# Kernel optimization log

Measured on AMD Instinct MI355X. Metric: run time of the kernel, lower is better.

The kernel has to match this reference:

```python
import jax, jax.numpy as jnp
import numpy as np

EMBED_DIM = 1024
NUM_HEADS = 16
HEAD_DIM = EMBED_DIM // NUM_HEADS
WINDOW = 3
N_RAND = 3
BLOCK = 64
BATCH = 2
SEQ = 2048


def _bigbird_mask(seq_len: int) -> np.ndarray:
    """Global + sliding-window + random block mask. True = attend.
    Deterministic (fixed numpy seed) stand-in for np.random.choice in the
    original; the mask is data-independent so it is a compile-time constant."""
    nb = -(-seq_len // BLOCK)  # ceil division
    mask = np.zeros((seq_len, seq_len), dtype=bool)
    g = min(BLOCK, seq_len)
    mask[:g, :] = True  # global rows
    mask[:, :g] = True  # global cols
    blk = np.arange(seq_len) // BLOCK
    # sliding window: block distance <= WINDOW (matches start/end block loop)
    mask |= np.abs(blk[:, None] - blk[None, :]) <= WINDOW
    rng = np.random.RandomState(0)
    for b in range(1, nb):
        avail = [x for x in range(1, nb) if abs(x - b) > WINDOW]
        if avail:
            sel = rng.choice(avail, size=min(N_RAND, len(avail)), replace=False)
            s0, s1 = b * BLOCK, min(seq_len, (b + 1) * BLOCK)
            for rb in sel:
                mask[s0:s1, rb * BLOCK:min(seq_len, (rb + 1) * BLOCK)] = True
    return mask


def setup_inputs() -> dict:
    key = jax.random.key(0)
    ks = jax.random.split(key, 9)
    E = EMBED_DIM
    std = E ** -0.5
    return {
        "hidden_states": jax.random.normal(ks[0], (BATCH, SEQ, E), jnp.float32),
        "wq": jax.random.normal(ks[1], (E, E), jnp.float32) * std,
        "bq": jnp.zeros((E,), jnp.float32),
        "wk": jax.random.normal(ks[2], (E, E), jnp.float32) * std,
        "bk": jnp.zeros((E,), jnp.float32),
        "wv": jax.random.normal(ks[3], (E, E), jnp.float32) * std,
        "bv": jnp.zeros((E,), jnp.float32),
        "wo": jax.random.normal(ks[4], (E, E), jnp.float32) * std,
        "bo": jnp.zeros((E,), jnp.float32),
    }


def reference(hidden_states, wq, bq, wk, bk, wv, bv, wo, bo):
    B, S, E = hidden_states.shape
    D = HEAD_DIM
    scale = D ** -0.5

    def proj(w, b):  # (B,S,E) -> (B,H,S,D)
        return (hidden_states @ w.T + b).reshape(B, S, NUM_HEADS, D).transpose(0, 2, 1, 3)

    q = proj(wq, bq)
    k = proj(wk, bk)
    v = proj(wv, bv)
    scores = jnp.einsum('bhqd,bhkd->bhqk', q, k) * scale  # dense, masked post-hoc (as in source)
    mask = jnp.asarray(_bigbird_mask(S))
    scores = jnp.where(mask[None, None, :, :], scores, -jnp.inf)
    attn = jax.nn.softmax(scores, axis=-1)
    out = jnp.einsum('bhqk,bhkd->bhqd', attn, v)
    out = out.transpose(0, 2, 1, 3).reshape(B, S, E)
    return out @ wo.T + bo
```

## Files before the change

### kernel.cpp

```cpp
#include <hip/hip_runtime.h>
#include <cstdint>
#include <math.h>


#define DEVI __device__ __forceinline__

typedef __bf16 bf16x8 __attribute__((ext_vector_type(8)));
typedef float floatx4 __attribute__((ext_vector_type(4)));
typedef unsigned short u16x8 __attribute__((ext_vector_type(8)));
typedef unsigned short u16x4 __attribute__((ext_vector_type(4)));
typedef unsigned short ushort_t;

typedef const __attribute__((address_space(1))) void* gptr_as1;
typedef __attribute__((address_space(3))) void* lptr_as3;

DEVI ushort_t f2bf(float f) {
  unsigned u = __float_as_uint(f);
  unsigned r = ((u >> 16) & 1u) + 0x7fffu;
  return (ushort_t)((u + r) >> 16);
}

DEVI void lds_load16(void* lds, const void* g) {
  __builtin_amdgcn_global_load_lds((gptr_as1)g, (lptr_as3)lds, 16, 0, 0);
}

DEVI floatx4 mfma16(bf16x8 a, bf16x8 b, floatx4 c) {
  return __builtin_amdgcn_mfma_f32_16x16x32_bf16(a, b, c, 0, 0, 0);
}

#define BARR() do { asm volatile("" ::: "memory"); \
                    __builtin_amdgcn_s_barrier();  \
                    asm volatile("" ::: "memory"); } while (0)
#define VMC(N) asm volatile("s_waitcnt vmcnt(" #N ")" ::: "memory")

struct MTState { unsigned mt[624]; int mti; };

constexpr unsigned mt_next(MTState& s) {
  if (s.mti >= 624) {
    for (int k = 0; k < 624; ++k) {
      unsigned y = (s.mt[k] & 0x80000000u) | (s.mt[(k + 1) % 624] & 0x7fffffffu);
      unsigned v = s.mt[(k + 397) % 624] ^ (y >> 1);
      if (y & 1u) v ^= 0x9908b0dfu;
      s.mt[k] = v;
    }
    s.mti = 0;
  }
  unsigned y = s.mt[s.mti++];
  y ^= y >> 11;
  y ^= (y << 7) & 0x9d2c5680u;
  y ^= (y << 15) & 0xefc60000u;
  y ^= y >> 18;
  return y;
}

constexpr unsigned mt_interval(MTState& s, unsigned mx) {
  if (mx == 0u) return 0u;
  unsigned msk = mx;
  msk |= msk >> 1; msk |= msk >> 2; msk |= msk >> 4; msk |= msk >> 8; msk |= msk >> 16;
  unsigned v = mt_next(s) & msk;
  while (v > mx) v = mt_next(s) & msk;
  return v;
}

struct MaskPack { unsigned char list[32][32]; int cnt[32]; };

constexpr MaskPack make_pack() {
  unsigned char m[32][32] = {};
  for (int i = 0; i < 32; ++i)
    for (int j = 0; j < 32; ++j) {
      int d = i - j; if (d < 0) d = -d;
      m[i][j] = (i == 0 || j == 0 || d <= 3) ? (unsigned char)1 : (unsigned char)0;
    }
  MTState st{};
  st.mt[0] = 0u;
  for (int i = 1; i < 624; ++i)
    st.mt[i] = 1812433253u * (st.mt[i - 1] ^ (st.mt[i - 1] >> 30)) + (unsigned)i;
  st.mti = 624;
  for (int b = 1; b < 32; ++b) {
    int avail[32] = {}; int n = 0;
    for (int x = 1; x < 32; ++x) {
      int d = x - b; if (d < 0) d = -d;
      if (d > 3) avail[n++] = x;
    }
    if (n == 0) continue;
    int perm[32] = {};
    for (int i = 0; i < n; ++i) perm[i] = i;
    for (int i = n - 1; i > 0; --i) {
      unsigned j = mt_interval(st, (unsigned)i);
      int t = perm[i]; perm[i] = perm[(int)j]; perm[(int)j] = t;
    }
    int take = n < 3 ? n : 3;
    for (int s = 0; s < take; ++s) m[b][avail[perm[s]]] = 1;
  }
  MaskPack P{};
  for (int i = 0; i < 32; ++i) {
    int c = 0;
    for (int j = 0; j < 32; ++j)
      if (m[i][j]) P.list[i][c++] = (unsigned char)j;
    P.cnt[i] = c;
  }
  return P;
}

__constant__ MaskPack MP = make_pack();

__global__ __launch_bounds__(256) void cvt_all(
    const float* __restrict__ hs, const float* __restrict__ wq,
    const float* __restrict__ wk, const float* __restrict__ wv,
    const float* __restrict__ wo,
    ushort_t* __restrict__ hs_bf, ushort_t* __restrict__ wq_bf,
    ushort_t* __restrict__ wk_bf, ushort_t* __restrict__ wv_bf,
    ushort_t* __restrict__ wo_bf) {
  const int i = blockIdx.x * 256 + threadIdx.x;
  const float* s;
  ushort_t* d;
  int j;
  if (i < 1048576) {
    s = hs; d = hs_bf; j = i;
  } else {
    const int t = (i - 1048576) >> 18;
    j = (i - 1048576) & 262143;
    s = t == 0 ? wq : (t == 1 ? wk : (t == 2 ? wv : wo));
    d = t == 0 ? wq_bf : (t == 1 ? wk_bf : (t == 2 ? wv_bf : wo_bf));
  }
  const float4 f = ((const float4*)s)[j];
  u16x4 o;
  o.x = f2bf(f.x); o.y = f2bf(f.y); o.z = f2bf(f.z); o.w = f2bf(f.w);
  ((u16x4*)d)[j] = o;
}

DEVI void stage_half(ushort_t* ldsb, const ushort_t* g, int w, int l) {
  lds_load16(ldsb + w * 1024 + l * 8, g);
  lds_load16(ldsb + w * 1024 + 512 + l * 8, g + 8192);
}

DEVI void rdA(bf16x8 (&a)[4][2], const ushort_t* base, int wm, int li, int quad) {
#pragma unroll
  for (int mi = 0; mi < 4; ++mi) {
    const int rh = wm * 64 + mi * 16 + li;
    const int sw = rh & 7;
#pragma unroll
    for (int ks = 0; ks < 2; ++ks)
      a[mi][ks] = *(const bf16x8*)(base + rh * 64 + (((ks * 4 + quad) ^ sw) << 3));
  }
}

DEVI void rdB(bf16x8 (&b)[2][2], const ushort_t* base, int wn, int li, int quad) {
#pragma unroll
  for (int ni = 0; ni < 2; ++ni) {
    const int rh = wn * 32 + ni * 16 + li;
    const int sw = rh & 7;
#pragma unroll
    for (int ks = 0; ks < 2; ++ks)
      b[ni][ks] = *(const bf16x8*)(base + rh * 64 + (((ks * 4 + quad) ^ sw) << 3));
  }
}

DEVI void mm16(floatx4 (&c)[4][2], const bf16x8 (&a)[4][2], const bf16x8 (&b)[2][2]) {
  __builtin_amdgcn_s_setprio(1);
#pragma unroll
  for (int ks = 0; ks < 2; ++ks)
#pragma unroll
    for (int mi = 0; mi < 4; ++mi)
#pragma unroll
      for (int ni = 0; ni < 2; ++ni)
        c[mi][ni] = mfma16(a[mi][ks], b[ni][ks], c[mi][ni]);
  __builtin_amdgcn_s_setprio(0);
}

__global__ __launch_bounds__(512, 2) void gemm_qkv_fused(
    const ushort_t* __restrict__ A,
    const ushort_t* __restrict__ W0, const ushort_t* __restrict__ W1,
    const ushort_t* __restrict__ W2,
    const float* __restrict__ bq, const float* __restrict__ bk,
    const float* __restrict__ bv,
    ushort_t* __restrict__ Qo, ushort_t* __restrict__ Ko,
    ushort_t* __restrict__ Vt) {
  __shared__ alignas(16) ushort_t LDS[2][2][2][8192];
  const int tid = threadIdx.x;
  const int w = tid >> 6, l = tid & 63, quad = l >> 4, li = l & 15;
  const int wm = w >> 2, wn = w & 3;
  const int bid = blockIdx.x;
  const int swz = (bid & 7) * 24 + (bid >> 3);
  const int m0 = (swz / 12) << 8;
  const int n0g = (swz % 12) << 8;
  const int z = n0g >> 10, n0l = n0g & 1023;
  const ushort_t* Bw = z == 0 ? W0 : (z == 1 ? W1 : W2);
  const float* bias = z == 0 ? bq : (z == 1 ? bk : bv);

  const int rst = w * 16 + (l >> 3);
  const int cst = ((l & 7) ^ (l >> 3)) << 3;
  const ushort_t* gA = A + (size_t)(m0 + rst) * 1024 + cst;
  const ushort_t* gB = Bw + (size_t)(n0l + rst) * 1024 + cst;

  const floatx4 fz = {0.0f, 0.0f, 0.0f, 0.0f};
  floatx4 acc[2][2][4][2];
#pragma unroll
  for (int qm = 0; qm < 2; ++qm)
#pragma unroll
    for (int qn = 0; qn < 2; ++qn)
#pragma unroll
      for (int mi = 0; mi < 4; ++mi)
#pragma unroll
        for (int ni = 0; ni < 2; ++ni) acc[qm][qn][mi][ni] = fz;

  bf16x8 a[4][2], b0[2][2], b1[2][2];

  stage_half(&LDS[0][0][0][0], gA, w, l);
  stage_half(&LDS[0][0][1][0], gA + 131072, w, l);
  stage_half(&LDS[0][1][0][0], gB, w, l);
  stage_half(&LDS[0][1][1][0], gB + 131072, w, l);
  stage_half(&LDS[1][0][0][0], gA + 64, w, l);
  stage_half(&LDS[1][1][0][0], gB + 64, w, l);
  stage_half(&LDS[1][1][1][0], gB + 131072 + 64, w, l);
  VMC(6);
  BARR();

#pragma unroll 1
  for (int it = 0; it < 8; ++it) {
    const bool pf = (it < 7);
    const int o_cy = (2 * it + 1) * 64;
    const int o_x = (2 * it + 2) * 64;
    const int o_y = (2 * it + 3) * 64;

    rdA(a, &LDS[0][0][0][0], wm, li, quad);
    rdB(b0, &LDS[0][1][0][0], wn, li, quad);
    stage_half(&LDS[1][0][1][0], gA + 131072 + o_cy, w, l);
    mm16(acc[0][0], a, b0);
    BARR();

    rdB(b1, &LDS[0][1][1][0], wn, li, quad);
    if (pf) stage_half(&LDS[0][0][0][0], gA + o_x, w, l);
    mm16(acc[0][1], a, b1);
    BARR();

    rdA(a, &LDS[0][0][1][0], wm, li, quad);
    if (pf) stage_half(&LDS[0][1][0][0], gB + o_x, w, l);
    mm16(acc[1][0], a, b0);
    BARR();

    if (pf) stage_half(&LDS[0][1][1][0], gB + 131072 + o_x, w, l);
    mm16(acc[1][1], a, b1);
    if (pf) { VMC(6); } else { VMC(0); }
    BARR();

    rdA(a, &LDS[1][0][0][0], wm, li, quad);
    rdB(b0, &LDS[1][1][0][0], wn, li, quad);
    if (pf) stage_half(&LDS[0][0][1][0], gA + 131072 + o_x, w, l);
    mm16(acc[0][0], a, b0);
    BARR();

    rdB(b1, &LDS[1][1][1][0], wn, li, quad);
    if (pf) stage_half(&LDS[1][0][0][0], gA + o_y, w, l);
    mm16(acc[0][1], a, b1);
    BARR();

    rdA(a, &LDS[1][0][1][0], wm, li, quad);
    if (pf) stage_half(&LDS[1][1][0][0], gB + o_y, w, l);
    mm16(acc[1][0], a, b0);
    BARR();

    if (pf) stage_half(&LDS[1][1][1][0], gB + 131072 + o_y, w, l);
    mm16(acc[1][1], a, b1);
    if (pf) { VMC(6); }
    BARR();
  }

#pragma unroll
  for (int Qm = 0; Qm < 2; ++Qm)
#pragma unroll
    for (int Qn = 0; Qn < 2; ++Qn)
#pragma unroll
      for (int ni = 0; ni < 2; ++ni) {
        const int col = n0l + Qn * 128 + wn * 32 + ni * 16 + li;
        const float bb_ = bias[col];
        if (z == 2) {
          const int hh = col >> 6, dd = col & 63;
#pragma unroll
          for (int mi = 0; mi < 4; ++mi) {
            const int row0 = m0 + Qm * 128 + wm * 64 + mi * 16 + quad * 4;
            const int bb = row0 >> 11, s0 = row0 & 2047;
            u16x4 pk;
#pragma unroll
            for (int r = 0; r < 4; ++r) pk[r] = f2bf(acc[Qm][Qn][mi][ni][r] + bb_);
            *(u16x4*)(Vt + (size_t)((bb * 16 + hh) * 64 + dd) * 2048 + s0) = pk;
          }
        } else {
          ushort_t* Co = (z == 0) ? Qo : Ko;
#pragma unroll
          for (int mi = 0; mi < 4; ++mi)
#pragma unroll
            for (int r = 0; r < 4; ++r) {
              const int row = m0 + Qm * 128 + wm * 64 + mi * 16 + quad * 4 + r;
              Co[(size_t)row * 1024 + col] = f2bf(acc[Qm][Qn][mi][ni][r] + bb_);
            }
        }
      }
}

__global__ __launch_bounds__(256) void gemm_o64(
    const ushort_t* __restrict__ A, const ushort_t* __restrict__ W,
    const float* __restrict__ bias, float* __restrict__ C) {
  constexpr int N = 1024, K = 1024;
  __shared__ alignas(16) ushort_t As[64 * 32];
  __shared__ alignas(16) ushort_t Bs[128 * 32];
  const int tid = threadIdx.x;
  const int w = tid >> 6, l = tid & 63, quad = l >> 4, li = l & 15;
  const int m0 = blockIdx.x * 64, n0 = blockIdx.y * 128;
  const int wm = (w >> 1) * 32, wn = (w & 1) * 64;

  const int lofA = w * 512 + l * 8;
  const int rA = lofA >> 5, cA = lofA & 31;
  const int lofB0 = (w * 2 + 0) * 512 + l * 8;
  const int lofB1 = (w * 2 + 1) * 512 + l * 8;
  const int rB0 = lofB0 >> 5, cB0 = lofB0 & 31;
  const int rB1 = lofB1 >> 5, cB1 = lofB1 & 31;
  const ushort_t* gA = A + (size_t)(m0 + rA) * K + cA;
  const ushort_t* gB0 = W + (size_t)(n0 + rB0) * K + cB0;
  const ushort_t* gB1 = W + (size_t)(n0 + rB1) * K + cB1;

  const floatx4 fzero = {0.0f, 0.0f, 0.0f, 0.0f};
  floatx4 acc[2][4];
#pragma unroll
  for (int i = 0; i < 2; ++i)
#pragma unroll
    for (int j = 0; j < 4; ++j) acc[i][j] = fzero;

  for (int k0 = 0; k0 < K; k0 += 32) {
    lds_load16(As + lofA, gA + k0);
    lds_load16(Bs + lofB0, gB0 + k0);
    lds_load16(Bs + lofB1, gB1 + k0);
    __syncthreads();
    bf16x8 af[2], bfr[4];
#pragma unroll
    for (int mi = 0; mi < 2; ++mi)
      af[mi] = *(const bf16x8*)(As + (wm + mi * 16 + li) * 32 + quad * 8);
#pragma unroll
    for (int ni = 0; ni < 4; ++ni)
      bfr[ni] = *(const bf16x8*)(Bs + (wn + ni * 16 + li) * 32 + quad * 8);
#pragma unroll
    for (int mi = 0; mi < 2; ++mi)
#pragma unroll
      for (int ni = 0; ni < 4; ++ni)
        acc[mi][ni] = mfma16(af[mi], bfr[ni], acc[mi][ni]);
    __syncthreads();
  }

#pragma unroll
  for (int ni = 0; ni < 4; ++ni) {
    const int col = n0 + wn + ni * 16 + li;
    const float bv = bias[col];
#pragma unroll
    for (int mi = 0; mi < 2; ++mi) {
#pragma unroll
      for (int r = 0; r < 4; ++r) {
        const int row = m0 + wm + mi * 16 + quad * 4 + r;
        C[(size_t)row * N + col] = acc[mi][ni][r] + bv;
      }
    }
  }
}

__global__ __launch_bounds__(256) void attn_kernel(
    const ushort_t* __restrict__ Q, const ushort_t* __restrict__ Kg,
    const ushort_t* __restrict__ Vtg, ushort_t* __restrict__ O,
    float* __restrict__ OP, float* __restrict__ LP) {
  __shared__ alignas(16) ushort_t Kls[64 * 72];
  __shared__ alignas(16) ushort_t Vls[64 * 72];
  __shared__ alignas(16) ushort_t Ps[4][16 * 72];

  const int tid = threadIdx.x;
  const int w = tid >> 6, l = tid & 63, quad = l >> 4, li = l & 15;
  const int hb = blockIdx.x;
  const int y = blockIdx.y;
  const bool partial = (y >= 31);
  const int qb = partial ? 0 : (y + 1);
  const int p = partial ? (y - 31) : 0;
  const int base = p * 11;
  const int nact = partial ? (32 - base < 11 ? 32 - base : 11) : MP.cnt[qb];

  const int h = hb & 15, b = hb >> 4;
  const size_t qoff = (size_t)b * 2048 * 1024 + (size_t)h * 64;
  const size_t vtoff = (size_t)hb * 64 * 2048;

  const int qrow = qb * 64 + w * 16 + li;
  bf16x8 aq0 = *(const bf16x8*)(Q + qoff + (size_t)qrow * 1024 + quad * 8);
  bf16x8 aq1 = *(const bf16x8*)(Q + qoff + (size_t)qrow * 1024 + 32 + quad * 8);
#pragma unroll
  for (int j = 0; j < 8; ++j) {
    aq0[j] = (__bf16)((float)aq0[j] * 0.125f);
    aq1[j] = (__bf16)((float)aq1[j] * 0.125f);
  }

  const floatx4 fzero = {0.0f, 0.0f, 0.0f, 0.0f};
  floatx4 o_acc[4];
  float lp[4];
#pragma unroll
  for (int nt = 0; nt < 4; ++nt) o_acc[nt] = fzero;
#pragma unroll
  for (int r = 0; r < 4; ++r) lp[r] = 0.0f;

  const int r0 = w * 16 + (l >> 3);
  const int r1 = r0 + 8;
  const int cb = (l & 7) * 8;
  const ushort_t* kg0 = Kg + qoff + (size_t)r0 * 1024 + cb;
  const ushort_t* kg1 = Kg + qoff + (size_t)r1 * 1024 + cb;
  const ushort_t* vg0 = Vtg + vtoff + (size_t)r0 * 2048 + cb;
  const ushort_t* vg1 = Vtg + vtoff + (size_t)r1 * 2048 + cb;
  ushort_t* kd0 = Kls + r0 * 72 + cb;
  ushort_t* kd1 = Kls + r1 * 72 + cb;
  ushort_t* vd0 = Vls + r0 * 72 + cb;
  ushort_t* vd1 = Vls + r1 * 72 + cb;
  ushort_t* PsW = Ps[w];

  int kb = MP.list[qb][base];
  {
    const u16x8 a0 = *(const u16x8*)(kg0 + (size_t)kb * 65536);
    const u16x8 a1 = *(const u16x8*)(kg1 + (size_t)kb * 65536);
    const u16x8 b0 = *(const u16x8*)(vg0 + kb * 64);
    const u16x8 b1 = *(const u16x8*)(vg1 + kb * 64);
    *(u16x8*)kd0 = a0; *(u16x8*)kd1 = a1;
    *(u16x8*)vd0 = b0; *(u16x8*)vd1 = b1;
  }

  for (int i = 0; i < nact; ++i) {
    const int kbn = (i + 1 < nact) ? (int)MP.list[qb][base + i + 1] : 0;
    __syncthreads();

    floatx4 s[4];
#pragma unroll
    for (int nt = 0; nt < 4; ++nt) {
      const bf16x8 bk0 = *(const bf16x8*)(Kls + (nt * 16 + li) * 72 + quad * 8);
      const bf16x8 bk1 = *(const bf16x8*)(Kls + (nt * 16 + li) * 72 + 32 + quad * 8);
      s[nt] = mfma16(aq1, bk1, mfma16(aq0, bk0, fzero));
    }

#pragma unroll
    for (int nt = 0; nt < 4; ++nt)
#pragma unroll
      for (int r = 0; r < 4; ++r) {
        const float e = __expf(s[nt][r]);
        lp[r] += e;
        PsW[(quad * 4 + r) * 72 + nt * 16 + li] = f2bf(e);
      }

#pragma unroll
    for (int c = 0; c < 2; ++c) {
      const bf16x8 pa = *(const bf16x8*)(PsW + li * 72 + c * 32 + quad * 8);
#pragma unroll
      for (int nt = 0; nt < 4; ++nt) {
        const bf16x8 vb = *(const bf16x8*)(Vls + (nt * 16 + li) * 72 + c * 32 + quad * 8);
        o_acc[nt] = mfma16(pa, vb, o_acc[nt]);
      }
    }

    __syncthreads();
    if (i + 1 < nact) {
      const u16x8 a0 = *(const u16x8*)(kg0 + (size_t)kbn * 65536);
      const u16x8 a1 = *(const u16x8*)(kg1 + (size_t)kbn * 65536);
      const u16x8 b0 = *(const u16x8*)(vg0 + kbn * 64);
      const u16x8 b1 = *(const u16x8*)(vg1 + kbn * 64);
      *(u16x8*)kd0 = a0; *(u16x8*)kd1 = a1;
      *(u16x8*)vd0 = b0; *(u16x8*)vd1 = b1;
    }
  }

#pragma unroll
  for (int stp = 1; stp <= 8; stp <<= 1)
#pragma unroll
    for (int r = 0; r < 4; ++r) lp[r] += __shfl_xor(lp[r], stp);

  if (!partial) {
#pragma unroll
    for (int r = 0; r < 4; ++r) {
      const float rinv = 1.0f / lp[r];
#pragma unroll
      for (int nt = 0; nt < 4; ++nt) {
        const float ov = o_acc[nt][r] * rinv;
        O[qoff + (size_t)(qb * 64 + w * 16 + quad * 4 + r) * 1024 + nt * 16 + li] = f2bf(ov);
      }
    }
  } else {
    float* O32 = OP + (size_t)(hb * 3 + p) * 4096;
    float* LPp = LP + (hb * 3 + p) * 64;
#pragma unroll
    for (int r = 0; r < 4; ++r) {
      const int row = w * 16 + quad * 4 + r;
#pragma unroll
      for (int nt = 0; nt < 4; ++nt)
        O32[row * 64 + nt * 16 + li] = o_acc[nt][r];
      if (li == 0) LPp[row] = lp[r];
    }
  }
}

__global__ __launch_bounds__(256) void combine_qb0(
    const float* __restrict__ OP, const float* __restrict__ LP,
    ushort_t* __restrict__ O) {
  const int hb = blockIdx.x;
  const int b = hb >> 4, h = hb & 15;
  const float* o0 = OP + (size_t)hb * 3 * 4096;
  const float* l0 = LP + hb * 3 * 64;
  for (int idx = threadIdx.x; idx < 4096; idx += 256) {
    const int q = idx >> 6, d = idx & 63;
    const float s = o0[idx] + o0[4096 + idx] + o0[8192 + idx];
    const float lsum = l0[q] + l0[64 + q] + l0[128 + q];
    O[(size_t)b * 2048 * 1024 + (size_t)q * 1024 + h * 64 + d] = f2bf(s / lsum);
  }
}

extern "C" void kernel_launch(void* const* d_in, const int* in_sizes, int n_in,
                              void* d_out, int out_size, void* d_ws, size_t ws_size,
                              hipStream_t stream) {
  const float* hs = (const float*)d_in[0];
  const float* wq = (const float*)d_in[1];
  const float* bq = (const float*)d_in[2];
  const float* wk = (const float*)d_in[3];
  const float* bk = (const float*)d_in[4];
  const float* wv = (const float*)d_in[5];
  const float* bv = (const float*)d_in[6];
  const float* wo = (const float*)d_in[7];
  const float* bo = (const float*)d_in[8];
  float* out = (float*)d_out;

  char* ws = (char*)d_ws;
  ushort_t* hs_bf = (ushort_t*)(ws);
  ushort_t* wq_bf = (ushort_t*)(ws + (8ull << 20));
  ushort_t* wk_bf = (ushort_t*)(ws + (10ull << 20));
  ushort_t* wv_bf = (ushort_t*)(ws + (12ull << 20));
  ushort_t* wo_bf = (ushort_t*)(ws + (14ull << 20));
  ushort_t* Qb = (ushort_t*)(ws + (16ull << 20));
  ushort_t* Kb = (ushort_t*)(ws + (24ull << 20));
  ushort_t* Vt = (ushort_t*)(ws + (32ull << 20));
  ushort_t* AO = hs_bf;
  float* OP = (float*)(ws + (10ull << 20));
  float* LP = (float*)((char*)OP + 32 * 3 * 4096 * sizeof(float));

  cvt_all<<<8192, 256, 0, stream>>>(hs, wq, wk, wv, wo,
                                    hs_bf, wq_bf, wk_bf, wv_bf, wo_bf);

  gemm_qkv_fused<<<192, 512, 0, stream>>>(hs_bf, wq_bf, wk_bf, wv_bf,
                                          bq, bk, bv, Qb, Kb, Vt);

  dim3 ga(32, 34, 1);
  attn_kernel<<<ga, 256, 0, stream>>>(Qb, Kb, Vt, AO, OP, LP);

  combine_qb0<<<32, 256, 0, stream>>>(OP, LP, AO);

  dim3 go(64, 8, 1);
  gemm_o64<<<go, 256, 0, stream>>>(AO, wo_bf, bo, out);
}
```

Measured before the change: 182.1 us.

## Retile QKV GEMM to 256x192 tiles and double-buffer output projection

The fused QKV GEMM moves from 192 blocks of 256x256 tiles to 256 blocks of 256x192 tiles, so the grid matches the CU count. Its complex half-step staging schedule is replaced by a plain double-buffered K loop with 64-wide steps, and it now handles tiles that cross the Q/K/V boundary per column. The output projection GEMM gains LDS double buffering, so the next K slice loads while the current one is multiplied, with one barrier per step. In exchange the QKV kernel loses its explicit occupancy hint, and each block holds more accumulator registers plus a larger LDS footprint.

```diff
diff --git a/kernel.cpp b/kernel.cpp
--- a/kernel.cpp
+++ b/kernel.cpp
@@ -134,41 +134,7 @@
   lds_load16(ldsb + w * 1024 + 512 + l * 8, g + 8192);
 }
 
-DEVI void rdA(bf16x8 (&a)[4][2], const ushort_t* base, int wm, int li, int quad) {
-#pragma unroll
-  for (int mi = 0; mi < 4; ++mi) {
-    const int rh = wm * 64 + mi * 16 + li;
-    const int sw = rh & 7;
-#pragma unroll
-    for (int ks = 0; ks < 2; ++ks)
-      a[mi][ks] = *(const bf16x8*)(base + rh * 64 + (((ks * 4 + quad) ^ sw) << 3));
-  }
-}
-
-DEVI void rdB(bf16x8 (&b)[2][2], const ushort_t* base, int wn, int li, int quad) {
-#pragma unroll
-  for (int ni = 0; ni < 2; ++ni) {
-    const int rh = wn * 32 + ni * 16 + li;
-    const int sw = rh & 7;
-#pragma unroll
-    for (int ks = 0; ks < 2; ++ks)
-      b[ni][ks] = *(const bf16x8*)(base + rh * 64 + (((ks * 4 + quad) ^ sw) << 3));
-  }
-}
-
-DEVI void mm16(floatx4 (&c)[4][2], const bf16x8 (&a)[4][2], const bf16x8 (&b)[2][2]) {
-  __builtin_amdgcn_s_setprio(1);
-#pragma unroll
-  for (int ks = 0; ks < 2; ++ks)
-#pragma unroll
-    for (int mi = 0; mi < 4; ++mi)
-#pragma unroll
-      for (int ni = 0; ni < 2; ++ni)
-        c[mi][ni] = mfma16(a[mi][ks], b[ni][ks], c[mi][ni]);
-  __builtin_amdgcn_s_setprio(0);
-}
-
-__global__ __launch_bounds__(512, 2) void gemm_qkv_fused(
+__global__ __launch_bounds__(512) void gemm_qkv_fused(
     const ushort_t* __restrict__ A,
     const ushort_t* __restrict__ W0, const ushort_t* __restrict__ W1,
     const ushort_t* __restrict__ W2,
@@ -176,134 +142,121 @@
     const float* __restrict__ bv,
     ushort_t* __restrict__ Qo, ushort_t* __restrict__ Ko,
     ushort_t* __restrict__ Vt) {
-  __shared__ alignas(16) ushort_t LDS[2][2][2][8192];
+  __shared__ alignas(16) ushort_t As[2][16384];
+  __shared__ alignas(16) ushort_t Bs[2][12288];
   const int tid = threadIdx.x;
   const int w = tid >> 6, l = tid & 63, quad = l >> 4, li = l & 15;
-  const int wm = w >> 2, wn = w & 3;
+  const int wm4 = w >> 1, wn2 = w & 1;
   const int bid = blockIdx.x;
-  const int swz = (bid & 7) * 24 + (bid >> 3);
-  const int m0 = (swz / 12) << 8;
-  const int n0g = (swz % 12) << 8;
-  const int z = n0g >> 10, n0l = n0g & 1023;
-  const ushort_t* Bw = z == 0 ? W0 : (z == 1 ? W1 : W2);
-  const float* bias = z == 0 ? bq : (z == 1 ? bk : bv);
-
-  const int rst = w * 16 + (l >> 3);
+  const int swz = (bid & 7) * 32 + (bid >> 3);
+  const int m0 = (swz >> 4) << 8;
+  const int n0g = (swz & 15) * 192;
+
   const int cst = ((l & 7) ^ (l >> 3)) << 3;
-  const ushort_t* gA = A + (size_t)(m0 + rst) * 1024 + cst;
-  const ushort_t* gB = Bw + (size_t)(n0l + rst) * 1024 + cst;
+  const int rstA = w * 16 + (l >> 3);
+  const ushort_t* gA = A + (size_t)(m0 + rstA) * 1024 + cst;
+  const ushort_t* gB[3];
+#pragma unroll
+  for (int s = 0; s < 3; ++s) {
+    const int brow = n0g + s * 64 + w * 8 + (l >> 3);
+    const int zs = brow >> 10, rs = brow & 1023;
+    const ushort_t* Wp = zs == 0 ? W0 : (zs == 1 ? W1 : W2);
+    gB[s] = Wp + (size_t)rs * 1024 + cst;
+  }
 
   const floatx4 fz = {0.0f, 0.0f, 0.0f, 0.0f};
-  floatx4 acc[2][2][4][2];
-#pragma unroll
-  for (int qm = 0; qm < 2; ++qm)
-#pragma unroll
-    for (int qn = 0; qn < 2; ++qn)
+  floatx4 acc[4][6];
+#pragma unroll
+  for (int mi = 0; mi < 4; ++mi)
+#pragma unroll
+    for (int ni = 0; ni < 6; ++ni) acc[mi][ni] = fz;
+
+  stage_half(&As[0][0], gA, w, l);
+  stage_half(&As[0][8192], gA + 131072, w, l);
+#pragma unroll
+  for (int s = 0; s < 3; ++s)
+    lds_load16(&Bs[0][s * 4096] + w * 512 + l * 8, gB[s]);
+  VMC(0);
+  BARR();
+
+#pragma unroll 1
+  for (int t = 0; t < 16; ++t) {
+    const int cur = t & 1;
+    const bool pf = (t + 1 < 16);
+    if (pf) {
+      const int k0 = (t + 1) * 64;
+      stage_half(&As[cur ^ 1][0], gA + k0, w, l);
+      stage_half(&As[cur ^ 1][8192], gA + 131072 + k0, w, l);
+#pragma unroll
+      for (int s = 0; s < 3; ++s)
+        lds_load16(&Bs[cur ^ 1][s * 4096] + w * 512 + l * 8, gB[s] + k0);
+    }
+
+    bf16x8 a[4][2], b[6][2];
+#pragma unroll
+    for (int mi = 0; mi < 4; ++mi) {
+      const int rh = wm4 * 64 + mi * 16 + li;
+      const int sw = rh & 7;
+#pragma unroll
+      for (int ks = 0; ks < 2; ++ks)
+        a[mi][ks] = *(const bf16x8*)(&As[cur][0] + rh * 64 + (((ks * 4 + quad) ^ sw) << 3));
+    }
+#pragma unroll
+    for (int ni = 0; ni < 6; ++ni) {
+      const int rh = wn2 * 96 + ni * 16 + li;
+      const int sw = rh & 7;
+#pragma unroll
+      for (int ks = 0; ks < 2; ++ks)
+        b[ni][ks] = *(const bf16x8*)(&Bs[cur][0] + rh * 64 + (((ks * 4 + quad) ^ sw) << 3));
+    }
+
+#pragma unroll
+    for (int ks = 0; ks < 2; ++ks)
 #pragma unroll
       for (int mi = 0; mi < 4; ++mi)
 #pragma unroll
-        for (int ni = 0; ni < 2; ++ni) acc[qm][qn][mi][ni] = fz;
-
-  bf16x8 a[4][2], b0[2][2], b1[2][2];
-
-  stage_half(&LDS[0][0][0][0], gA, w, l);
-  stage_half(&LDS[0][0][1][0], gA + 131072, w, l);
-  stage_half(&LDS[0][1][0][0], gB, w, l);
-  stage_half(&LDS[0][1][1][0], gB + 131072, w, l);
-  stage_half(&LDS[1][0][0][0], gA + 64, w, l);
-  stage_half(&LDS[1][1][0][0], gB + 64, w, l);
-  stage_half(&LDS[1][1][1][0], gB + 131072 + 64, w, l);
-  VMC(6);
-  BARR();
-
-#pragma unroll 1
-  for (int it = 0; it < 8; ++it) {
-    const bool pf = (it < 7);
-    const int o_cy = (2 * it + 1) * 64;
-    const int o_x = (2 * it + 2) * 64;
-    const int o_y = (2 * it + 3) * 64;
-
-    rdA(a, &LDS[0][0][0][0], wm, li, quad);
-    rdB(b0, &LDS[0][1][0][0], wn, li, quad);
-    stage_half(&LDS[1][0][1][0], gA + 131072 + o_cy, w, l);
-    mm16(acc[0][0], a, b0);
-    BARR();
-
-    rdB(b1, &LDS[0][1][1][0], wn, li, quad);
-    if (pf) stage_half(&LDS[0][0][0][0], gA + o_x, w, l);
-    mm16(acc[0][1], a, b1);
-    BARR();
-
-    rdA(a, &LDS[0][0][1][0], wm, li, quad);
-    if (pf) stage_half(&LDS[0][1][0][0], gB + o_x, w, l);
-    mm16(acc[1][0], a, b0);
-    BARR();
-
-    if (pf) stage_half(&LDS[0][1][1][0], gB + 131072 + o_x, w, l);
-    mm16(acc[1][1], a, b1);
-    if (pf) { VMC(6); } else { VMC(0); }
-    BARR();
-
-    rdA(a, &LDS[1][0][0][0], wm, li, quad);
-    rdB(b0, &LDS[1][1][0][0], wn, li, quad);
-    if (pf) stage_half(&LDS[0][0][1][0], gA + 131072 + o_x, w, l);
-    mm16(acc[0][0], a, b0);
-    BARR();
-
-    rdB(b1, &LDS[1][1][1][0], wn, li, quad);
-    if (pf) stage_half(&LDS[1][0][0][0], gA + o_y, w, l);
-    mm16(acc[0][1], a, b1);
-    BARR();
-
-    rdA(a, &LDS[1][0][1][0], wm, li, quad);
-    if (pf) stage_half(&LDS[1][1][0][0], gB + o_y, w, l);
-    mm16(acc[1][0], a, b0);
-    BARR();
-
-    if (pf) stage_half(&LDS[1][1][1][0], gB + 131072 + o_y, w, l);
-    mm16(acc[1][1], a, b1);
-    if (pf) { VMC(6); }
-    BARR();
-  }
-
-#pragma unroll
-  for (int Qm = 0; Qm < 2; ++Qm)
-#pragma unroll
-    for (int Qn = 0; Qn < 2; ++Qn)
-#pragma unroll
-      for (int ni = 0; ni < 2; ++ni) {
-        const int col = n0l + Qn * 128 + wn * 32 + ni * 16 + li;
-        const float bb_ = bias[col];
-        if (z == 2) {
-          const int hh = col >> 6, dd = col & 63;
-#pragma unroll
-          for (int mi = 0; mi < 4; ++mi) {
-            const int row0 = m0 + Qm * 128 + wm * 64 + mi * 16 + quad * 4;
-            const int bb = row0 >> 11, s0 = row0 & 2047;
-            u16x4 pk;
-#pragma unroll
-            for (int r = 0; r < 4; ++r) pk[r] = f2bf(acc[Qm][Qn][mi][ni][r] + bb_);
-            *(u16x4*)(Vt + (size_t)((bb * 16 + hh) * 64 + dd) * 2048 + s0) = pk;
-          }
-        } else {
-          ushort_t* Co = (z == 0) ? Qo : Ko;
-#pragma unroll
-          for (int mi = 0; mi < 4; ++mi)
-#pragma unroll
-            for (int r = 0; r < 4; ++r) {
-              const int row = m0 + Qm * 128 + wm * 64 + mi * 16 + quad * 4 + r;
-              Co[(size_t)row * 1024 + col] = f2bf(acc[Qm][Qn][mi][ni][r] + bb_);
-            }
+        for (int ni = 0; ni < 6; ++ni)
+          acc[mi][ni] = mfma16(a[mi][ks], b[ni][ks], acc[mi][ni]);
+
+    if (pf) { VMC(0); BARR(); }
+  }
+
+#pragma unroll
+  for (int ni = 0; ni < 6; ++ni) {
+    const int col = n0g + wn2 * 96 + ni * 16 + li;
+    const int zc = col >> 10, coll = col & 1023;
+    const float* bias = zc == 0 ? bq : (zc == 1 ? bk : bv);
+    const float bb_ = bias[coll];
+    if (zc == 2) {
+      const int hh = coll >> 6, dd = coll & 63;
+#pragma unroll
+      for (int mi = 0; mi < 4; ++mi) {
+        const int row0 = m0 + wm4 * 64 + mi * 16 + quad * 4;
+        const int bb = row0 >> 11, s0 = row0 & 2047;
+        u16x4 pk;
+#pragma unroll
+        for (int r = 0; r < 4; ++r) pk[r] = f2bf(acc[mi][ni][r] + bb_);
+        *(u16x4*)(Vt + (size_t)((bb * 16 + hh) * 64 + dd) * 2048 + s0) = pk;
+      }
+    } else {
+      ushort_t* Co = (zc == 0) ? Qo : Ko;
+#pragma unroll
+      for (int mi = 0; mi < 4; ++mi)
+#pragma unroll
+        for (int r = 0; r < 4; ++r) {
+          const int row = m0 + wm4 * 64 + mi * 16 + quad * 4 + r;
+          Co[(size_t)row * 1024 + coll] = f2bf(acc[mi][ni][r] + bb_);
         }
-      }
+    }
+  }
 }
 
 __global__ __launch_bounds__(256) void gemm_o64(
     const ushort_t* __restrict__ A, const ushort_t* __restrict__ W,
     const float* __restrict__ bias, float* __restrict__ C) {
   constexpr int N = 1024, K = 1024;
-  __shared__ alignas(16) ushort_t As[64 * 32];
-  __shared__ alignas(16) ushort_t Bs[128 * 32];
+  __shared__ alignas(16) ushort_t As[2][64 * 32];
+  __shared__ alignas(16) ushort_t Bs[2][128 * 32];
   const int tid = threadIdx.x;
   const int w = tid >> 6, l = tid & 63, quad = l >> 4, li = l & 15;
   const int m0 = blockIdx.x * 64, n0 = blockIdx.y * 128;
@@ -326,24 +279,35 @@
 #pragma unroll
     for (int j = 0; j < 4; ++j) acc[i][j] = fzero;
 
-  for (int k0 = 0; k0 < K; k0 += 32) {
-    lds_load16(As + lofA, gA + k0);
-    lds_load16(Bs + lofB0, gB0 + k0);
-    lds_load16(Bs + lofB1, gB1 + k0);
-    __syncthreads();
+  lds_load16(&As[0][0] + lofA, gA);
+  lds_load16(&Bs[0][0] + lofB0, gB0);
+  lds_load16(&Bs[0][0] + lofB1, gB1);
+  VMC(0);
+  BARR();
+
+#pragma unroll 1
+  for (int it = 0; it < 32; ++it) {
+    const int cur = it & 1;
+    const bool pf = (it + 1 < 32);
+    if (pf) {
+      const int k0 = (it + 1) * 32;
+      lds_load16(&As[cur ^ 1][0] + lofA, gA + k0);
+      lds_load16(&Bs[cur ^ 1][0] + lofB0, gB0 + k0);
+      lds_load16(&Bs[cur ^ 1][0] + lofB1, gB1 + k0);
+    }
     bf16x8 af[2], bfr[4];
 #pragma unroll
     for (int mi = 0; mi < 2; ++mi)
-      af[mi] = *(const bf16x8*)(As + (wm + mi * 16 + li) * 32 + quad * 8);
+      af[mi] = *(const bf16x8*)(&As[cur][0] + (wm + mi * 16 + li) * 32 + quad * 8);
 #pragma unroll
     for (int ni = 0; ni < 4; ++ni)
-      bfr[ni] = *(const bf16x8*)(Bs + (wn + ni * 16 + li) * 32 + quad * 8);
+      bfr[ni] = *(const bf16x8*)(&Bs[cur][0] + (wn + ni * 16 + li) * 32 + quad * 8);
 #pragma unroll
     for (int mi = 0; mi < 2; ++mi)
 #pragma unroll
       for (int ni = 0; ni < 4; ++ni)
         acc[mi][ni] = mfma16(af[mi], bfr[ni], acc[mi][ni]);
-    __syncthreads();
+    if (pf) { VMC(0); BARR(); }
   }
 
 #pragma unroll
@@ -539,7 +503,7 @@
   cvt_all<<<8192, 256, 0, stream>>>(hs, wq, wk, wv, wo,
                                     hs_bf, wq_bf, wk_bf, wv_bf, wo_bf);
 
-  gemm_qkv_fused<<<192, 512, 0, stream>>>(hs_bf, wq_bf, wk_bf, wv_bf,
+  gemm_qkv_fused<<<256, 512, 0, stream>>>(hs_bf, wq_bf, wk_bf, wv_bf,
                                           bq, bk, bv, Qb, Kb, Vt);
 
   dim3 ga(32, 34, 1);
```

After: 185.3 us. About the same (+1.7%).
